# Kernel tuning notes

Measured on AMD Instinct MI355X. Metric: run time of the kernel, lower is better.

The kernel has to match this reference:

```python
import jax, jax.numpy as jnp
import numpy as np

T, B, E, H = 2048, 2, 1024, 16
D = E // H  # head_dim = 64


def setup_inputs() -> dict:
    key = jax.random.key(0)
    ks = jax.random.split(key, 5)
    s = 1.0 / np.sqrt(E)  # keep projections well-scaled like xavier init
    return {
        "query": jax.random.normal(ks[0], (T, B, E), jnp.float32),
        "Wq": jax.random.normal(ks[1], (E, E), jnp.float32) * s,
        "bq": jnp.zeros((E,), jnp.float32),
        "Wk": jax.random.normal(ks[2], (E, E), jnp.float32) * s,
        "bk": jnp.zeros((E,), jnp.float32),
        "Wv": jax.random.normal(ks[3], (E, E), jnp.float32) * s,
        "bv": jnp.zeros((E,), jnp.float32),
        "Wo": jax.random.normal(ks[4], (E, E), jnp.float32) * s,
        "bo": jnp.zeros((E,), jnp.float32),
    }


def reference(query, Wq, bq, Wk, bk, Wv, bv, Wo, bo):
    # query: [T, B, E] (seq_len, batch, embed_dim), fairseq layout
    scaling = D ** -0.5
    q = (query @ Wq.T + bq) * scaling           # [T, B, E]
    k = query @ Wk.T + bk                       # [T, B, E] (self-attention)
    v = query @ Wv.T + bv                       # [T, B, E]
    # split heads: [T, B, H, D]
    q = q.reshape(T, B, H, D)
    k = k.reshape(T, B, H, D)
    v = v.reshape(T, B, H, D)
    # attention scores [B, H, T, S] (S == T, no masks, global window)
    scores = jnp.einsum("tbhd,sbhd->bhts", q, k)
    probs = jax.nn.softmax(scores, axis=-1)     # dropout p=0 -> identity
    attn = jnp.einsum("bhts,sbhd->tbhd", probs, v).reshape(T, B, E)
    return attn @ Wo.T + bo                     # [T, B, E]
```

## Files before the change

kernel.cpp:

```cpp
#include <hip/hip_runtime.h>
#include <hip/hip_bf16.h>
#include <stdint.h>


#define T_SEQ 2048
#define BATCH 2
#define EMB   1024
#define NH    16
#define HD    64
#define N_X   (T_SEQ * BATCH * EMB)
#define N_W   (EMB * EMB)

typedef short s16;
typedef s16   bf16x8 __attribute__((ext_vector_type(8)));
typedef float f32x4  __attribute__((ext_vector_type(4)));

__device__ __forceinline__ f32x4 mfma16(bf16x8 a, bf16x8 b, f32x4 c) {
  return __builtin_amdgcn_mfma_f32_16x16x32_bf16(a, b, c, 0, 0, 0);
}

__device__ __forceinline__ void gload16(const void* g, void* l) {
  __builtin_amdgcn_global_load_lds(
      (const __attribute__((address_space(1))) uint32_t*)g,
      (__attribute__((address_space(3))) uint32_t*)l, 16, 0, 0);
}

__device__ __forceinline__ s16 f2b(float x) {
  return (s16)__builtin_bit_cast(unsigned short, __float2bfloat16(x));
}

__device__ __forceinline__ uint32_t pk2(float lo, float hi) {
  float2 f; f.x = lo; f.y = hi;
  __hip_bfloat162 h = __float22bfloat162_rn(f);
  const uint32_t xl = (uint32_t)__builtin_bit_cast(unsigned short, h.x);
  const uint32_t xh = (uint32_t)__builtin_bit_cast(unsigned short, h.y);
  return (xh << 16) | xl;
}

__device__ __forceinline__ bf16x8 cvt8(const float* p) {
  f32x4 a = *(const f32x4*)p;
  f32x4 b = *(const f32x4*)(p + 4);
  bf16x8 r;
  r[0] = f2b(a[0]); r[1] = f2b(a[1]); r[2] = f2b(a[2]); r[3] = f2b(a[3]);
  r[4] = f2b(b[0]); r[5] = f2b(b[1]); r[6] = f2b(b[2]); r[7] = f2b(b[3]);
  return r;
}

__global__ __launch_bounds__(256)
void convert_kernel(const float* __restrict__ X, const float* __restrict__ Wq,
                    const float* __restrict__ Wk, const float* __restrict__ Wv,
                    const float* __restrict__ Wo,
                    s16* __restrict__ dst, s16* __restrict__ Wob)
{
  const int idx = (blockIdx.x * 256 + threadIdx.x) * 8;
  if (idx < N_X) {
    *(bf16x8*)&dst[idx] = cvt8(X + idx);
  } else if (idx < N_X + 3 * N_W) {
    const int r = idx - N_X;
    const int w = r >> 20;
    const float* src = (w == 0) ? Wq : (w == 1) ? Wk : Wv;
    *(bf16x8*)&dst[idx] = cvt8(src + (r & (N_W - 1)));
  } else {
    const int off = idx - (N_X + 3 * N_W);
    *(bf16x8*)&Wob[off] = cvt8(Wo + off);
  }
}

__global__ __launch_bounds__(256)
void gemm_qkv_kernel(const s16* __restrict__ Xb,
                     const s16* __restrict__ Wb,
                     const float* __restrict__ bq, const float* __restrict__ bk,
                     const float* __restrict__ bv,
                     __hip_bfloat16* __restrict__ Qh, __hip_bfloat16* __restrict__ Kh,
                     s16* __restrict__ Vt)
{
  __shared__ __align__(16) s16 lA[128 * 32];
  __shared__ __align__(16) s16 lB[128 * 32];
  const int tid  = threadIdx.x;
  const int lane = tid & 63;
  const int wave = tid >> 6;
  const int which = blockIdx.y >> 3;
  const s16* W = Wb + (size_t)which * N_W;
  const float* bias = (which == 0) ? bq : (which == 1) ? bk : bv;
  const int m0 = blockIdx.x * 128;
  const int n0 = (blockIdx.y & 7) * 128;
  const int srow = tid >> 2;
  const int scol = (tid & 3) * 8;
  const int wr = (wave >> 1) * 64;
  const int wc = (wave & 1) * 64;
  const int fr = lane & 15;
  const int fk = (lane >> 4) * 8;

  f32x4 acc[4][4] = {};

  for (int k0 = 0; k0 < EMB; k0 += 32) {
    gload16(Xb + (size_t)(m0 + srow) * EMB + k0 + scol,      &lA[srow * 32 + scol]);
    gload16(Xb + (size_t)(m0 + 64 + srow) * EMB + k0 + scol, &lA[(64 + srow) * 32 + scol]);
    gload16(W + (size_t)(n0 + srow) * EMB + k0 + scol,       &lB[srow * 32 + scol]);
    gload16(W + (size_t)(n0 + 64 + srow) * EMB + k0 + scol,  &lB[(64 + srow) * 32 + scol]);
    __syncthreads();
    bf16x8 af[4], bfr[4];
#pragma unroll
    for (int i = 0; i < 4; ++i) af[i]  = *(const bf16x8*)&lA[(wr + i * 16 + fr) * 32 + fk];
#pragma unroll
    for (int i = 0; i < 4; ++i) bfr[i] = *(const bf16x8*)&lB[(wc + i * 16 + fr) * 32 + fk];
#pragma unroll
    for (int mi = 0; mi < 4; ++mi)
#pragma unroll
      for (int ni = 0; ni < 4; ++ni)
        acc[mi][ni] = mfma16(af[mi], bfr[ni], acc[mi][ni]);
    __syncthreads();
  }

  const float scale = (which == 0) ? 0.125f * 1.44269504088896f : 1.0f;
  __hip_bfloat16* Y = (which == 0) ? Qh : Kh;
  const int fq = lane >> 4;
#pragma unroll
  for (int mi = 0; mi < 4; ++mi) {
#pragma unroll
    for (int ni = 0; ni < 4; ++ni) {
      const int nn = n0 + wc + ni * 16 + fr;
      const float bb = bias[nn];
      const int h = nn >> 6, d = nn & 63;
#pragma unroll
      for (int r = 0; r < 4; ++r) {
        const int m = m0 + wr + mi * 16 + fq * 4 + r;
        const int t = m >> 1, b = m & 1;
        const float y = (acc[mi][ni][r] + bb) * scale;
        if (which == 2) {
          const int tl = t & 31;
          const int tp = ((tl & 12) << 1) + (tl & 3) + ((tl >> 4) << 2);
          Vt[(((size_t)b * NH + h) * HD + d) * T_SEQ + (t & ~31) + tp] = f2b(y);
        } else {
          Y[(((size_t)b * NH + h) * T_SEQ + t) * HD + d] = __float2bfloat16(y);
        }
      }
    }
  }
}

__global__ __launch_bounds__(256)
void gemm_out_bf16_kernel(const s16* __restrict__ X,
                          const s16* __restrict__ Wb,
                          const float* __restrict__ bias,
                          float* __restrict__ Y)
{
  __shared__ __align__(16) s16 lA[128 * 32];
  __shared__ __align__(16) s16 lB[128 * 32];
  const int tid  = threadIdx.x;
  const int lane = tid & 63;
  const int wave = tid >> 6;
  const int m0 = blockIdx.x * 128;
  const int n0 = blockIdx.y * 128;
  const int srow = tid >> 2;
  const int scol = (tid & 3) * 8;
  const int wr = (wave >> 1) * 64;
  const int wc = (wave & 1) * 64;
  const int fr = lane & 15;
  const int fk = (lane >> 4) * 8;

  f32x4 acc[4][4] = {};

  for (int k0 = 0; k0 < EMB; k0 += 32) {
    gload16(X + (size_t)(m0 + srow) * EMB + k0 + scol,       &lA[srow * 32 + scol]);
    gload16(X + (size_t)(m0 + 64 + srow) * EMB + k0 + scol,  &lA[(64 + srow) * 32 + scol]);
    gload16(Wb + (size_t)(n0 + srow) * EMB + k0 + scol,      &lB[srow * 32 + scol]);
    gload16(Wb + (size_t)(n0 + 64 + srow) * EMB + k0 + scol, &lB[(64 + srow) * 32 + scol]);
    __syncthreads();
    bf16x8 af[4], bfr[4];
#pragma unroll
    for (int i = 0; i < 4; ++i) af[i]  = *(const bf16x8*)&lA[(wr + i * 16 + fr) * 32 + fk];
#pragma unroll
    for (int i = 0; i < 4; ++i) bfr[i] = *(const bf16x8*)&lB[(wc + i * 16 + fr) * 32 + fk];
#pragma unroll
    for (int mi = 0; mi < 4; ++mi)
#pragma unroll
      for (int ni = 0; ni < 4; ++ni)
        acc[mi][ni] = mfma16(af[mi], bfr[ni], acc[mi][ni]);
    __syncthreads();
  }

  const int fq = lane >> 4;
#pragma unroll
  for (int mi = 0; mi < 4; ++mi) {
#pragma unroll
    for (int ni = 0; ni < 4; ++ni) {
      const int nn = n0 + wc + ni * 16 + fr;
      const float bb = bias[nn];
#pragma unroll
      for (int r = 0; r < 4; ++r) {
        const int m = m0 + wr + mi * 16 + fq * 4 + r;
        Y[(size_t)m * EMB + nn] = acc[mi][ni][r] + bb;
      }
    }
  }
}

__global__ __launch_bounds__(256)
void gemm_out_kernel(const s16* __restrict__ X,
                     const float* __restrict__ W,
                     const float* __restrict__ bias,
                     float* __restrict__ Y)
{
  __shared__ __align__(16) s16 lA[128 * 32];
  __shared__ __align__(16) s16 lB[128 * 32];
  const int tid  = threadIdx.x;
  const int lane = tid & 63;
  const int wave = tid >> 6;
  const int m0 = blockIdx.x * 128;
  const int n0 = blockIdx.y * 128;
  const int srow = tid >> 2;
  const int scol = (tid & 3) * 8;
  const int wr = (wave >> 1) * 64;
  const int wc = (wave & 1) * 64;
  const int fr = lane & 15;
  const int fk = (lane >> 4) * 8;

  f32x4 acc[4][4] = {};

  for (int k0 = 0; k0 < EMB; k0 += 32) {
    gload16(X + (size_t)(m0 + srow) * EMB + k0 + scol,      &lA[srow * 32 + scol]);
    gload16(X + (size_t)(m0 + 64 + srow) * EMB + k0 + scol, &lA[(64 + srow) * 32 + scol]);
    bf16x8 b0 = cvt8(W + (size_t)(n0 + srow) * EMB + k0 + scol);
    bf16x8 b1 = cvt8(W + (size_t)(n0 + 64 + srow) * EMB + k0 + scol);
    *(bf16x8*)&lB[srow * 32 + scol] = b0;
    *(bf16x8*)&lB[(64 + srow) * 32 + scol] = b1;
    __syncthreads();
    bf16x8 af[4], bfr[4];
#pragma unroll
    for (int i = 0; i < 4; ++i) af[i]  = *(const bf16x8*)&lA[(wr + i * 16 + fr) * 32 + fk];
#pragma unroll
    for (int i = 0; i < 4; ++i) bfr[i] = *(const bf16x8*)&lB[(wc + i * 16 + fr) * 32 + fk];
#pragma unroll
    for (int mi = 0; mi < 4; ++mi)
#pragma unroll
      for (int ni = 0; ni < 4; ++ni)
        acc[mi][ni] = mfma16(af[mi], bfr[ni], acc[mi][ni]);
    __syncthreads();
  }

  const int fq = lane >> 4;
#pragma unroll
  for (int mi = 0; mi < 4; ++mi) {
#pragma unroll
    for (int ni = 0; ni < 4; ++ni) {
      const int nn = n0 + wc + ni * 16 + fr;
      const float bb = bias[nn];
#pragma unroll
      for (int r = 0; r < 4; ++r) {
        const int m = m0 + wr + mi * 16 + fq * 4 + r;
        Y[(size_t)m * EMB + nn] = acc[mi][ni][r] + bb;
      }
    }
  }
}

__global__ __launch_bounds__(256, 4)
void attn_kernel(const s16* __restrict__ Qh,
                 const s16* __restrict__ Kh,
                 const s16* __restrict__ Vt,
                 __hip_bfloat16* __restrict__ attn)
{
  __shared__ __align__(16) s16 lK[2][64 * 64];
  __shared__ __align__(16) s16 lV[2][64 * 64];
  const int tid  = threadIdx.x;
  const int lane = tid & 63;
  const int wave = tid >> 6;

  const int lid = blockIdx.x;
  const int nid = (lid & 7) * 128 + (lid >> 3);
  const int qb = nid & 31;
  const int bh = nid >> 5;

  const int q0 = qb * 64 + wave * 16;
  const size_t baseK = (size_t)bh * T_SEQ * HD;
  const size_t baseV = (size_t)bh * HD * T_SEQ;
  const int fr = lane & 15;
  const int fq = lane >> 4;
  const int fk = fq * 8;
  const int xk = fr & 7;

  const int srow  = tid >> 3;
  const int scol  = (tid & 7) * 8;
  const int scolK = (((tid & 7) ^ ((tid >> 3) & 7)) * 8);

  const bf16x8 qf0 = *(const bf16x8*)&Qh[baseK + (size_t)(q0 + fr) * HD + fk];
  const bf16x8 qf1 = *(const bf16x8*)&Qh[baseK + (size_t)(q0 + fr) * HD + 32 + fk];

  union { uint32_t u[4]; bf16x8 v; } ones;
  ones.u[0] = ones.u[1] = ones.u[2] = ones.u[3] = 0x3F803F80u;

  f32x4 o_acc[4] = {};
  f32x4 l_acc = {};

  auto stage = [&](int b, int sB) {
    gload16(Kh + baseK + (size_t)(sB + srow) * HD + scolK,         &lK[b][srow * 64 + scol]);
    gload16(Kh + baseK + (size_t)(sB + 32 + srow) * HD + scolK,    &lK[b][(32 + srow) * 64 + scol]);
    gload16(Vt + baseV + (size_t)srow * T_SEQ + sB + scolK,        &lV[b][srow * 64 + scol]);
    gload16(Vt + baseV + (size_t)(32 + srow) * T_SEQ + sB + scolK, &lV[b][(32 + srow) * 64 + scol]);
  };

  stage(0, 0);

  for (int t = 0; t < T_SEQ / 64; ++t) {
    const int cur = t & 1;
    __syncthreads();
    if (t + 1 < T_SEQ / 64) stage(cur ^ 1, (t + 1) * 64);

    const s16* kb = lK[cur];
    const s16* vb = lV[cur];

    f32x4 s_acc[4];
    __builtin_amdgcn_s_setprio(1);
#pragma unroll
    for (int sc = 0; sc < 4; ++sc) {
      const int row = (sc * 16 + fr) * 64;
      bf16x8 kf0 = *(const bf16x8*)&kb[row + ((fq ^ xk) << 3)];
      bf16x8 kf1 = *(const bf16x8*)&kb[row + (((fq + 4) ^ xk) << 3)];
      f32x4 z = {-8.f, -8.f, -8.f, -8.f};
      z = mfma16(kf0, qf0, z);
      z = mfma16(kf1, qf1, z);
      s_acc[sc] = z;
    }
    __builtin_amdgcn_s_setprio(0);

    bf16x8 vf[2][4];
#pragma unroll
    for (int h = 0; h < 2; ++h)
#pragma unroll
      for (int dn = 0; dn < 4; ++dn)
        vf[h][dn] = *(const bf16x8*)&vb[(dn * 16 + fr) * 64 + (((h * 4 + fq) ^ xk) << 3)];

    uint32_t w[4][2];
#pragma unroll
    for (int sc = 0; sc < 4; ++sc) {
      const float p0 = __builtin_amdgcn_exp2f(s_acc[sc][0]);
      const float p1 = __builtin_amdgcn_exp2f(s_acc[sc][1]);
      const float p2 = __builtin_amdgcn_exp2f(s_acc[sc][2]);
      const float p3 = __builtin_amdgcn_exp2f(s_acc[sc][3]);
      w[sc][0] = pk2(p0, p1);
      w[sc][1] = pk2(p2, p3);
    }

    __builtin_amdgcn_s_setprio(1);
#pragma unroll
    for (int h = 0; h < 2; ++h) {
      union { uint32_t u[4]; bf16x8 v; } pa;
      pa.u[0] = w[2 * h][0];     pa.u[1] = w[2 * h][1];
      pa.u[2] = w[2 * h + 1][0]; pa.u[3] = w[2 * h + 1][1];
      l_acc = mfma16(pa.v, ones.v, l_acc);
#pragma unroll
      for (int dn = 0; dn < 4; ++dn)
        o_acc[dn] = mfma16(pa.v, vf[h][dn], o_acc[dn]);
    }
    __builtin_amdgcn_s_setprio(0);
  }

  const int b = bh >> 4, h = bh & 15;
#pragma unroll
  for (int r = 0; r < 4; ++r) {
    const int t = q0 + fq * 4 + r;
    const float linv = 1.0f / l_acc[r];
#pragma unroll
    for (int dn = 0; dn < 4; ++dn) {
      const int d = dn * 16 + fr;
      attn[((size_t)t * BATCH + b) * EMB + h * HD + d] =
          __float2bfloat16(o_acc[dn][r] * linv);
    }
  }
}

extern "C" void kernel_launch(void* const* d_in, const int* in_sizes, int n_in,
                              void* d_out, int out_size, void* d_ws, size_t ws_size,
                              hipStream_t stream) {
  const float* query = (const float*)d_in[0];
  const float* Wq = (const float*)d_in[1];
  const float* bq = (const float*)d_in[2];
  const float* Wk = (const float*)d_in[3];
  const float* bk = (const float*)d_in[4];
  const float* Wv = (const float*)d_in[5];
  const float* bv = (const float*)d_in[6];
  const float* Wo = (const float*)d_in[7];
  const float* bo = (const float*)d_in[8];

  char* ws = (char*)d_ws;
  const size_t SZ = (size_t)BATCH * NH * T_SEQ * HD * sizeof(s16);
  __hip_bfloat16* Qh = (__hip_bfloat16*)(ws);
  __hip_bfloat16* Kh = (__hip_bfloat16*)(ws + SZ);
  __hip_bfloat16* attnb = (__hip_bfloat16*)(ws + 2 * SZ);
  s16* Vt = (s16*)(ws + 3 * SZ);
  s16* Wob = (s16*)(ws + 4 * SZ);
  const bool useWob = ws_size >= 4 * SZ + (size_t)N_W * sizeof(s16);

  s16* Xb = (s16*)d_out;
  s16* Wb = Xb + (size_t)N_X;

  const int convN = N_X + 3 * N_W + (useWob ? N_W : 0);
  dim3 blk(256);
  convert_kernel<<<dim3(convN / 2048), blk, 0, stream>>>(query, Wq, Wk, Wv, Wo, Xb,
                                                         useWob ? Wob : (s16*)Xb);
  gemm_qkv_kernel<<<dim3(32, 24), blk, 0, stream>>>(Xb, Wb, bq, bk, bv, Qh, Kh, Vt);
  attn_kernel<<<dim3(1024), blk, 0, stream>>>((const s16*)Qh, (const s16*)Kh, Vt, attnb);
  if (useWob)
    gemm_out_bf16_kernel<<<dim3(32, 8), blk, 0, stream>>>((const s16*)attnb, (const s16*)Wob,
                                                          bo, (float*)d_out);
  else
    gemm_out_kernel<<<dim3(32, 8), blk, 0, stream>>>((const s16*)attnb, Wo, bo, (float*)d_out);
}
```

Measured before the change: 121.3 us.

## Process two 16-row query tiles per wave in attention with 128-thread blocks

The attention kernel now uses 2 waves per block instead of 4, with each wave handling 32 query rows as two 16-row sub-tiles that share every K and V fragment read from LDS. This halves LDS fragment reads per unit of MFMA work, and the staging loop is rewritten so 128 threads still fill the 64x64 K/V tiles. In exchange each wave holds roughly twice the accumulator and score registers, and fewer waves per block may leave less parallelism for hiding latency.

```diff
diff --git a/kernel.cpp b/kernel.cpp
--- a/kernel.cpp
+++ b/kernel.cpp
@@ -255,7 +255,7 @@
   }
 }
 
-__global__ __launch_bounds__(256, 4)
+__global__ __launch_bounds__(128)
 void attn_kernel(const s16* __restrict__ Qh,
                  const s16* __restrict__ Kh,
                  const s16* __restrict__ Vt,
@@ -272,7 +272,7 @@
   const int qb = nid & 31;
   const int bh = nid >> 5;
 
-  const int q0 = qb * 64 + wave * 16;
+  const int q0 = qb * 64 + wave * 32;
   const size_t baseK = (size_t)bh * T_SEQ * HD;
   const size_t baseV = (size_t)bh * HD * T_SEQ;
   const int fr = lane & 15;
@@ -280,24 +280,28 @@
   const int fk = fq * 8;
   const int xk = fr & 7;
 
-  const int srow  = tid >> 3;
-  const int scol  = (tid & 7) * 8;
-  const int scolK = (((tid & 7) ^ ((tid >> 3) & 7)) * 8);
-
-  const bf16x8 qf0 = *(const bf16x8*)&Qh[baseK + (size_t)(q0 + fr) * HD + fk];
-  const bf16x8 qf1 = *(const bf16x8*)&Qh[baseK + (size_t)(q0 + fr) * HD + 32 + fk];
+  const int srow0 = wave * 8 + (lane >> 3);
+  const int scg   = lane & 7;
+  const int sgc   = (scg ^ (srow0 & 7)) << 3;
+
+  const bf16x8 qa0 = *(const bf16x8*)&Qh[baseK + (size_t)(q0 + fr) * HD + fk];
+  const bf16x8 qa1 = *(const bf16x8*)&Qh[baseK + (size_t)(q0 + fr) * HD + 32 + fk];
+  const bf16x8 qb0 = *(const bf16x8*)&Qh[baseK + (size_t)(q0 + 16 + fr) * HD + fk];
+  const bf16x8 qb1 = *(const bf16x8*)&Qh[baseK + (size_t)(q0 + 16 + fr) * HD + 32 + fk];
 
   union { uint32_t u[4]; bf16x8 v; } ones;
   ones.u[0] = ones.u[1] = ones.u[2] = ones.u[3] = 0x3F803F80u;
 
-  f32x4 o_acc[4] = {};
-  f32x4 l_acc = {};
+  f32x4 oa[4] = {}, ob[4] = {};
+  f32x4 la = {}, lb = {};
 
   auto stage = [&](int b, int sB) {
-    gload16(Kh + baseK + (size_t)(sB + srow) * HD + scolK,         &lK[b][srow * 64 + scol]);
-    gload16(Kh + baseK + (size_t)(sB + 32 + srow) * HD + scolK,    &lK[b][(32 + srow) * 64 + scol]);
-    gload16(Vt + baseV + (size_t)srow * T_SEQ + sB + scolK,        &lV[b][srow * 64 + scol]);
-    gload16(Vt + baseV + (size_t)(32 + srow) * T_SEQ + sB + scolK, &lV[b][(32 + srow) * 64 + scol]);
+#pragma unroll
+    for (int j = 0; j < 4; ++j) {
+      const int row = j * 16 + srow0;
+      gload16(Kh + baseK + (size_t)(sB + row) * HD + sgc, &lK[b][row * 64 + scg * 8]);
+      gload16(Vt + baseV + (size_t)row * T_SEQ + sB + sgc, &lV[b][row * 64 + scg * 8]);
+    }
   };
 
   stage(0, 0);
@@ -310,7 +314,7 @@
     const s16* kb = lK[cur];
     const s16* vb = lV[cur];
 
-    f32x4 s_acc[4];
+    f32x4 za[4], zb[4];
     __builtin_amdgcn_s_setprio(1);
 #pragma unroll
     for (int sc = 0; sc < 4; ++sc) {
@@ -318,9 +322,13 @@
       bf16x8 kf0 = *(const bf16x8*)&kb[row + ((fq ^ xk) << 3)];
       bf16x8 kf1 = *(const bf16x8*)&kb[row + (((fq + 4) ^ xk) << 3)];
       f32x4 z = {-8.f, -8.f, -8.f, -8.f};
-      z = mfma16(kf0, qf0, z);
-      z = mfma16(kf1, qf1, z);
-      s_acc[sc] = z;
+      z = mfma16(kf0, qa0, z);
+      z = mfma16(kf1, qa1, z);
+      za[sc] = z;
+      f32x4 y = {-8.f, -8.f, -8.f, -8.f};
+      y = mfma16(kf0, qb0, y);
+      y = mfma16(kf1, qb1, y);
+      zb[sc] = y;
     }
     __builtin_amdgcn_s_setprio(0);
 
@@ -331,27 +339,30 @@
       for (int dn = 0; dn < 4; ++dn)
         vf[h][dn] = *(const bf16x8*)&vb[(dn * 16 + fr) * 64 + (((h * 4 + fq) ^ xk) << 3)];
 
-    uint32_t w[4][2];
+    uint32_t wa[4][2], wb[4][2];
 #pragma unroll
     for (int sc = 0; sc < 4; ++sc) {
-      const float p0 = __builtin_amdgcn_exp2f(s_acc[sc][0]);
-      const float p1 = __builtin_amdgcn_exp2f(s_acc[sc][1]);
-      const float p2 = __builtin_amdgcn_exp2f(s_acc[sc][2]);
-      const float p3 = __builtin_amdgcn_exp2f(s_acc[sc][3]);
-      w[sc][0] = pk2(p0, p1);
-      w[sc][1] = pk2(p2, p3);
+      wa[sc][0] = pk2(__builtin_amdgcn_exp2f(za[sc][0]), __builtin_amdgcn_exp2f(za[sc][1]));
+      wa[sc][1] = pk2(__builtin_amdgcn_exp2f(za[sc][2]), __builtin_amdgcn_exp2f(za[sc][3]));
+      wb[sc][0] = pk2(__builtin_amdgcn_exp2f(zb[sc][0]), __builtin_amdgcn_exp2f(zb[sc][1]));
+      wb[sc][1] = pk2(__builtin_amdgcn_exp2f(zb[sc][2]), __builtin_amdgcn_exp2f(zb[sc][3]));
     }
 
     __builtin_amdgcn_s_setprio(1);
 #pragma unroll
     for (int h = 0; h < 2; ++h) {
-      union { uint32_t u[4]; bf16x8 v; } pa;
-      pa.u[0] = w[2 * h][0];     pa.u[1] = w[2 * h][1];
-      pa.u[2] = w[2 * h + 1][0]; pa.u[3] = w[2 * h + 1][1];
-      l_acc = mfma16(pa.v, ones.v, l_acc);
-#pragma unroll
-      for (int dn = 0; dn < 4; ++dn)
-        o_acc[dn] = mfma16(pa.v, vf[h][dn], o_acc[dn]);
+      union { uint32_t u[4]; bf16x8 v; } pa, pb;
+      pa.u[0] = wa[2 * h][0];     pa.u[1] = wa[2 * h][1];
+      pa.u[2] = wa[2 * h + 1][0]; pa.u[3] = wa[2 * h + 1][1];
+      pb.u[0] = wb[2 * h][0];     pb.u[1] = wb[2 * h][1];
+      pb.u[2] = wb[2 * h + 1][0]; pb.u[3] = wb[2 * h + 1][1];
+      la = mfma16(pa.v, ones.v, la);
+      lb = mfma16(pb.v, ones.v, lb);
+#pragma unroll
+      for (int dn = 0; dn < 4; ++dn) {
+        oa[dn] = mfma16(pa.v, vf[h][dn], oa[dn]);
+        ob[dn] = mfma16(pb.v, vf[h][dn], ob[dn]);
+      }
     }
     __builtin_amdgcn_s_setprio(0);
   }
@@ -359,13 +370,15 @@
   const int b = bh >> 4, h = bh & 15;
 #pragma unroll
   for (int r = 0; r < 4; ++r) {
-    const int t = q0 + fq * 4 + r;
-    const float linv = 1.0f / l_acc[r];
+    const int ta = q0 + fq * 4 + r;
+    const int tb = ta + 16;
+    const float lia = 1.0f / la[r];
+    const float lib = 1.0f / lb[r];
 #pragma unroll
     for (int dn = 0; dn < 4; ++dn) {
       const int d = dn * 16 + fr;
-      attn[((size_t)t * BATCH + b) * EMB + h * HD + d] =
-          __float2bfloat16(o_acc[dn][r] * linv);
+      attn[((size_t)ta * BATCH + b) * EMB + h * HD + d] = __float2bfloat16(oa[dn][r] * lia);
+      attn[((size_t)tb * BATCH + b) * EMB + h * HD + d] = __float2bfloat16(ob[dn][r] * lib);
     }
   }
 }
@@ -400,7 +413,7 @@
   convert_kernel<<<dim3(convN / 2048), blk, 0, stream>>>(query, Wq, Wk, Wv, Wo, Xb,
                                                          useWob ? Wob : (s16*)Xb);
   gemm_qkv_kernel<<<dim3(32, 24), blk, 0, stream>>>(Xb, Wb, bq, bk, bv, Qh, Kh, Vt);
-  attn_kernel<<<dim3(1024), blk, 0, stream>>>((const s16*)Qh, (const s16*)Kh, Vt, attnb);
+  attn_kernel<<<dim3(1024), dim3(128), 0, stream>>>((const s16*)Qh, (const s16*)Kh, Vt, attnb);
   if (useWob)
     gemm_out_bf16_kernel<<<dim3(32, 8), blk, 0, stream>>>((const s16*)attnb, (const s16*)Wob,
                                                           bo, (float*)d_out);
```

Result: slower. 128.0 us (+5.5%).

## Use 32x32 MFMA in attention with split-K waves and LDS reduction

Applied to the files above, without the earlier changes.

Switches the attention inner loop from 16x16x32 to 32x32x16 bf16 MFMA tiles. Each wave now owns a 32-query block and half of each 64-key tile, so two waves share queries and their partial outputs and row sums are combined through LDS at the end. The V transpose permutation in the projection epilogue changes to match the new P-operand register layout. This cuts LDS fragment loads per FLOP and uses the larger MFMA shape, at the cost of a 16-wide accumulator per wave, an extra LDS reduction with two barriers, and half the waves idle during the final store.

```diff
diff --git a/kernel.cpp b/kernel.cpp
--- a/kernel.cpp
+++ b/kernel.cpp
@@ -14,9 +14,13 @@
 typedef short s16;
 typedef s16   bf16x8 __attribute__((ext_vector_type(8)));
 typedef float f32x4  __attribute__((ext_vector_type(4)));
+typedef float f32x16 __attribute__((ext_vector_type(16)));
 
 __device__ __forceinline__ f32x4 mfma16(bf16x8 a, bf16x8 b, f32x4 c) {
   return __builtin_amdgcn_mfma_f32_16x16x32_bf16(a, b, c, 0, 0, 0);
+}
+__device__ __forceinline__ f32x16 mfma32(bf16x8 a, bf16x8 b, f32x16 c) {
+  return __builtin_amdgcn_mfma_f32_32x32x16_bf16(a, b, c, 0, 0, 0);
 }
 
 __device__ __forceinline__ void gload16(const void* g, void* l) {
@@ -129,7 +133,7 @@
         const float y = (acc[mi][ni][r] + bb) * scale;
         if (which == 2) {
           const int tl = t & 31;
-          const int tp = ((tl & 12) << 1) + (tl & 3) + ((tl >> 4) << 2);
+          const int tp = (tl & ~12) | (((tl >> 2) & 1) << 3) | (((tl >> 3) & 1) << 2);
           Vt[(((size_t)b * NH + h) * HD + d) * T_SEQ + (t & ~31) + tp] = f2b(y);
         } else {
           Y[(((size_t)b * NH + h) * T_SEQ + t) * HD + d] = __float2bfloat16(y);
@@ -261,43 +265,45 @@
                  const s16* __restrict__ Vt,
                  __hip_bfloat16* __restrict__ attn)
 {
-  __shared__ __align__(16) s16 lK[2][64 * 64];
-  __shared__ __align__(16) s16 lV[2][64 * 64];
+  __shared__ __align__(16) s16 lmem[4 * 64 * 64];
+  s16* lK0 = lmem;
+  s16* lV0 = lmem + 2 * 64 * 64;
   const int tid  = threadIdx.x;
   const int lane = tid & 63;
   const int wave = tid >> 6;
+  const int qhalf = wave >> 1;
+  const int khalf = wave & 1;
 
   const int lid = blockIdx.x;
   const int nid = (lid & 7) * 128 + (lid >> 3);
   const int qb = nid & 31;
   const int bh = nid >> 5;
 
-  const int q0 = qb * 64 + wave * 16;
+  const int q0 = qb * 64 + qhalf * 32;
   const size_t baseK = (size_t)bh * T_SEQ * HD;
   const size_t baseV = (size_t)bh * HD * T_SEQ;
-  const int fr = lane & 15;
-  const int fq = lane >> 4;
-  const int fk = fq * 8;
-  const int xk = fr & 7;
+  const int ln = lane & 31;
+  const int lu = lane >> 5;
 
   const int srow  = tid >> 3;
   const int scol  = (tid & 7) * 8;
   const int scolK = (((tid & 7) ^ ((tid >> 3) & 7)) * 8);
 
-  const bf16x8 qf0 = *(const bf16x8*)&Qh[baseK + (size_t)(q0 + fr) * HD + fk];
-  const bf16x8 qf1 = *(const bf16x8*)&Qh[baseK + (size_t)(q0 + fr) * HD + 32 + fk];
+  bf16x8 qf[4];
+#pragma unroll
+  for (int ks = 0; ks < 4; ++ks)
+    qf[ks] = *(const bf16x8*)&Qh[baseK + (size_t)(q0 + ln) * HD + ks * 16 + lu * 8];
 
   union { uint32_t u[4]; bf16x8 v; } ones;
   ones.u[0] = ones.u[1] = ones.u[2] = ones.u[3] = 0x3F803F80u;
 
-  f32x4 o_acc[4] = {};
-  f32x4 l_acc = {};
+  f32x16 o0 = {}, o1 = {}, l_acc = {};
 
   auto stage = [&](int b, int sB) {
-    gload16(Kh + baseK + (size_t)(sB + srow) * HD + scolK,         &lK[b][srow * 64 + scol]);
-    gload16(Kh + baseK + (size_t)(sB + 32 + srow) * HD + scolK,    &lK[b][(32 + srow) * 64 + scol]);
-    gload16(Vt + baseV + (size_t)srow * T_SEQ + sB + scolK,        &lV[b][srow * 64 + scol]);
-    gload16(Vt + baseV + (size_t)(32 + srow) * T_SEQ + sB + scolK, &lV[b][(32 + srow) * 64 + scol]);
+    gload16(Kh + baseK + (size_t)(sB + srow) * HD + scolK,         &lK0[b * 4096 + srow * 64 + scol]);
+    gload16(Kh + baseK + (size_t)(sB + 32 + srow) * HD + scolK,    &lK0[b * 4096 + (32 + srow) * 64 + scol]);
+    gload16(Vt + baseV + (size_t)srow * T_SEQ + sB + scolK,        &lV0[b * 4096 + srow * 64 + scol]);
+    gload16(Vt + baseV + (size_t)(32 + srow) * T_SEQ + sB + scolK, &lV0[b * 4096 + (32 + srow) * 64 + scol]);
   };
 
   stage(0, 0);
@@ -307,65 +313,102 @@
     __syncthreads();
     if (t + 1 < T_SEQ / 64) stage(cur ^ 1, (t + 1) * 64);
 
-    const s16* kb = lK[cur];
-    const s16* vb = lV[cur];
-
-    f32x4 s_acc[4];
+    const s16* kb = lK0 + cur * 4096;
+    const s16* vb = lV0 + cur * 4096;
+
+    f32x16 s_acc;
+#pragma unroll
+    for (int i = 0; i < 16; ++i) s_acc[i] = -8.f;
+    const int krow = khalf * 32 + ln;
+    const int kswz = krow & 7;
     __builtin_amdgcn_s_setprio(1);
 #pragma unroll
-    for (int sc = 0; sc < 4; ++sc) {
-      const int row = (sc * 16 + fr) * 64;
-      bf16x8 kf0 = *(const bf16x8*)&kb[row + ((fq ^ xk) << 3)];
-      bf16x8 kf1 = *(const bf16x8*)&kb[row + (((fq + 4) ^ xk) << 3)];
-      f32x4 z = {-8.f, -8.f, -8.f, -8.f};
-      z = mfma16(kf0, qf0, z);
-      z = mfma16(kf1, qf1, z);
-      s_acc[sc] = z;
+    for (int ks = 0; ks < 4; ++ks) {
+      bf16x8 kf = *(const bf16x8*)&kb[krow * 64 + (((ks * 2 + lu) ^ kswz) << 3)];
+      s_acc = mfma32(kf, qf[ks], s_acc);
     }
     __builtin_amdgcn_s_setprio(0);
 
-    bf16x8 vf[2][4];
-#pragma unroll
-    for (int h = 0; h < 2; ++h)
-#pragma unroll
-      for (int dn = 0; dn < 4; ++dn)
-        vf[h][dn] = *(const bf16x8*)&vb[(dn * 16 + fr) * 64 + (((h * 4 + fq) ^ xk) << 3)];
-
-    uint32_t w[4][2];
-#pragma unroll
-    for (int sc = 0; sc < 4; ++sc) {
-      const float p0 = __builtin_amdgcn_exp2f(s_acc[sc][0]);
-      const float p1 = __builtin_amdgcn_exp2f(s_acc[sc][1]);
-      const float p2 = __builtin_amdgcn_exp2f(s_acc[sc][2]);
-      const float p3 = __builtin_amdgcn_exp2f(s_acc[sc][3]);
-      w[sc][0] = pk2(p0, p1);
-      w[sc][1] = pk2(p2, p3);
+    bf16x8 vf[2][2];
+#pragma unroll
+    for (int db = 0; db < 2; ++db) {
+      const int vrow = db * 32 + ln;
+      const int vswz = vrow & 7;
+#pragma unroll
+      for (int j = 0; j < 2; ++j)
+        vf[db][j] = *(const bf16x8*)&vb[vrow * 64 + (((khalf * 4 + j * 2 + lu) ^ vswz) << 3)];
+    }
+
+    uint32_t pw[8];
+#pragma unroll
+    for (int i = 0; i < 8; ++i) {
+      const float e0 = __builtin_amdgcn_exp2f(s_acc[2 * i]);
+      const float e1 = __builtin_amdgcn_exp2f(s_acc[2 * i + 1]);
+      pw[i] = pk2(e0, e1);
     }
 
     __builtin_amdgcn_s_setprio(1);
 #pragma unroll
-    for (int h = 0; h < 2; ++h) {
+    for (int j = 0; j < 2; ++j) {
       union { uint32_t u[4]; bf16x8 v; } pa;
-      pa.u[0] = w[2 * h][0];     pa.u[1] = w[2 * h][1];
-      pa.u[2] = w[2 * h + 1][0]; pa.u[3] = w[2 * h + 1][1];
-      l_acc = mfma16(pa.v, ones.v, l_acc);
-#pragma unroll
-      for (int dn = 0; dn < 4; ++dn)
-        o_acc[dn] = mfma16(pa.v, vf[h][dn], o_acc[dn]);
+      pa.u[0] = pw[j * 4 + 0]; pa.u[1] = pw[j * 4 + 1];
+      pa.u[2] = pw[j * 4 + 2]; pa.u[3] = pw[j * 4 + 3];
+      l_acc = mfma32(pa.v, ones.v, l_acc);
+      o0 = mfma32(pa.v, vf[0][j], o0);
+      o1 = mfma32(pa.v, vf[1][j], o1);
     }
     __builtin_amdgcn_s_setprio(0);
   }
 
-  const int b = bh >> 4, h = bh & 15;
-#pragma unroll
-  for (int r = 0; r < 4; ++r) {
-    const int t = q0 + fq * 4 + r;
-    const float linv = 1.0f / l_acc[r];
-#pragma unroll
-    for (int dn = 0; dn < 4; ++dn) {
-      const int d = dn * 16 + fr;
-      attn[((size_t)t * BATCH + b) * EMB + h * HD + d] =
-          __float2bfloat16(o_acc[dn][r] * linv);
+  __syncthreads();
+  float* cb = reinterpret_cast<float*>(lmem);
+  float* my = cb + (size_t)((qhalf << 6) + lane) * 52;
+  if (khalf == 1) {
+#pragma unroll
+    for (int c = 0; c < 4; ++c) {
+      f32x4 v;
+      v[0] = o0[4 * c]; v[1] = o0[4 * c + 1]; v[2] = o0[4 * c + 2]; v[3] = o0[4 * c + 3];
+      *(f32x4*)&my[4 * c] = v;
+    }
+#pragma unroll
+    for (int c = 0; c < 4; ++c) {
+      f32x4 v;
+      v[0] = o1[4 * c]; v[1] = o1[4 * c + 1]; v[2] = o1[4 * c + 2]; v[3] = o1[4 * c + 3];
+      *(f32x4*)&my[16 + 4 * c] = v;
+    }
+#pragma unroll
+    for (int c = 0; c < 4; ++c) {
+      f32x4 v;
+      v[0] = l_acc[4 * c]; v[1] = l_acc[4 * c + 1]; v[2] = l_acc[4 * c + 2]; v[3] = l_acc[4 * c + 3];
+      *(f32x4*)&my[32 + 4 * c] = v;
+    }
+  }
+  __syncthreads();
+  if (khalf == 0) {
+#pragma unroll
+    for (int c = 0; c < 4; ++c) {
+      f32x4 v = *(const f32x4*)&my[4 * c];
+      o0[4 * c] += v[0]; o0[4 * c + 1] += v[1]; o0[4 * c + 2] += v[2]; o0[4 * c + 3] += v[3];
+    }
+#pragma unroll
+    for (int c = 0; c < 4; ++c) {
+      f32x4 v = *(const f32x4*)&my[16 + 4 * c];
+      o1[4 * c] += v[0]; o1[4 * c + 1] += v[1]; o1[4 * c + 2] += v[2]; o1[4 * c + 3] += v[3];
+    }
+#pragma unroll
+    for (int c = 0; c < 4; ++c) {
+      f32x4 v = *(const f32x4*)&my[32 + 4 * c];
+      l_acc[4 * c] += v[0]; l_acc[4 * c + 1] += v[1]; l_acc[4 * c + 2] += v[2]; l_acc[4 * c + 3] += v[3];
+    }
+
+    const int b = bh >> 4, h = bh & 15;
+#pragma unroll
+    for (int r = 0; r < 16; ++r) {
+      const int q = (r & 3) + 8 * (r >> 2) + 4 * lu;
+      const int t = q0 + q;
+      const float linv = 1.0f / l_acc[r];
+      attn[((size_t)t * BATCH + b) * EMB + h * HD + ln]      = __float2bfloat16(o0[r] * linv);
+      attn[((size_t)t * BATCH + b) * EMB + h * HD + 32 + ln] = __float2bfloat16(o1[r] * linv);
     }
   }
 }
```

Result: slower. 136.7 us (+12.7%).
